# Optimization experiments

Measured on AMD Instinct MI355X. Metric: run time of the kernel, lower is better.

The kernel has to match this reference:

```python
import jax, jax.numpy as jnp
import numpy as np

HIDDEN = 1024

def setup_inputs() -> dict:
    key = jax.random.key(0)
    k1, k2, k3 = jax.random.split(key, 3)
    X = jax.random.normal(k1, (4, 2048, HIDDEN), dtype=jnp.float32)
    W = jax.random.normal(k2, (HIDDEN, 3 * HIDDEN), dtype=jnp.float32) * (1.0 / np.sqrt(HIDDEN))
    b = jax.random.normal(k3, (3 * HIDDEN,), dtype=jnp.float32) * 0.02
    return {"X": X, "W": W, "b": b}

def reference(X, W, b):
    D = X.shape[-1]
    # fused QKV projection: [B,S,3D]
    QKV = jnp.einsum('bsd,de->bse', X, W) + b
    Q, K, V = jnp.split(QKV, 3, axis=-1)
    # full attention scores [B,S,S]
    scores = jnp.einsum('bqd,bkd->bqk', Q, K) / jnp.sqrt(jnp.float32(D))
    attn = jax.nn.softmax(scores, axis=-1)
    out = jnp.einsum('bqk,bkd->bqd', attn, V)
    return out
```

## Files before the change

kernel.cpp:

```cpp
#include <hip/hip_runtime.h>

typedef unsigned short u16;
typedef unsigned int   u32;
typedef __attribute__((ext_vector_type(8)))  short bf16x8;
typedef __attribute__((ext_vector_type(16))) float f32x16;
typedef __attribute__((ext_vector_type(4)))  unsigned short us4;

__device__ __forceinline__ u16 f2bf(float f) {
    union { float f; u32 u; } v; v.f = f;
    u32 u = v.u;
    return (u16)((u + 0x7fffu + ((u >> 16) & 1u)) >> 16);
}
__device__ __forceinline__ float bf2f_lo(u32 p) {
    union { u32 u; float f; } t; t.u = p << 16; return t.f;
}
__device__ __forceinline__ float bf2f_hi(u32 p) {
    union { u32 u; float f; } t; t.u = p & 0xffff0000u; return t.f;
}

__device__ __forceinline__ void gload_lds16(const void* g, void* l) {
    __builtin_amdgcn_global_load_lds((const __attribute__((address_space(1))) u32*)g,
                                     (__attribute__((address_space(3))) u32*)l,
                                     16, 0, 0);
}

template<bool OUT_BF16, bool ADD_BIAS>
__global__ __launch_bounds__(256)
void gemm_bt(const u16* __restrict__ A, int lda, size_t strA,
             const u16* __restrict__ B, int ldb, size_t strB,
             void* __restrict__ Cv, int ldc, size_t strC,
             const float* __restrict__ bias, int K, float alpha)
{
    __shared__ __align__(16) u16 As[128 * 32];
    __shared__ __align__(16) u16 Bs[128 * 32];

    const int tid  = threadIdx.x;
    const int w    = tid >> 6;
    const int lane = tid & 63;
    const int wm   = w >> 1, wn = w & 1;
    const int m0   = blockIdx.y * 128, n0 = blockIdx.x * 128;
    const int l31  = lane & 31, lh = lane >> 5;

    A += (size_t)blockIdx.z * strA;
    B += (size_t)blockIdx.z * strB;

    size_t goffA[2], goffB[2];
#pragma unroll
    for (int h = 0; h < 2; ++h) {
        const int c = h * 256 + w * 64 + lane;
        const int r = c >> 2;
        const int q = ((c & 3) - (r >> 1)) & 3;
        goffA[h] = (size_t)(m0 + r) * lda + q * 8;
        goffB[h] = (size_t)(n0 + r) * ldb + q * 8;
    }

    int offA[2][2], offB[2][2];
#pragma unroll
    for (int i = 0; i < 2; ++i) {
        const int ra = wm * 64 + i * 32 + l31;
        const int rb = wn * 64 + i * 32 + l31;
#pragma unroll
        for (int ks = 0; ks < 2; ++ks) {
            const int qq = ks * 2 + lh;
            offA[i][ks] = (ra * 4 + ((qq + (ra >> 1)) & 3)) * 16;
            offB[i][ks] = (rb * 4 + ((qq + (rb >> 1)) & 3)) * 16;
        }
    }

    f32x16 acc[2][2] = {};

    for (int k0 = 0; k0 < K; k0 += 32) {
        gload_lds16(A + goffA[0] + k0, (char*)As + (w * 64) * 16);
        gload_lds16(A + goffA[1] + k0, (char*)As + (256 + w * 64) * 16);
        gload_lds16(B + goffB[0] + k0, (char*)Bs + (w * 64) * 16);
        gload_lds16(B + goffB[1] + k0, (char*)Bs + (256 + w * 64) * 16);
        __syncthreads();

        bf16x8 af[2][2], bfr[2][2];
#pragma unroll
        for (int i = 0; i < 2; ++i)
#pragma unroll
            for (int ks = 0; ks < 2; ++ks) {
                af[i][ks]  = *(const bf16x8*)((const char*)As + offA[i][ks]);
                bfr[i][ks] = *(const bf16x8*)((const char*)Bs + offB[i][ks]);
            }
#pragma unroll
        for (int ks = 0; ks < 2; ++ks)
#pragma unroll
            for (int i = 0; i < 2; ++i)
#pragma unroll
                for (int j = 0; j < 2; ++j)
                    acc[i][j] = __builtin_amdgcn_mfma_f32_32x32x16_bf16(
                        af[i][ks], bfr[j][ks], acc[i][j], 0, 0, 0);
        __syncthreads();
    }

    float bval[2];
    if (ADD_BIAS) {
#pragma unroll
        for (int j = 0; j < 2; ++j) bval[j] = bias[n0 + wn * 64 + j * 32 + l31];
    }
#pragma unroll
    for (int i = 0; i < 2; ++i) {
        const int rowb = m0 + wm * 64 + i * 32 + 4 * lh;
#pragma unroll
        for (int j = 0; j < 2; ++j) {
            const int col = n0 + wn * 64 + j * 32 + l31;
#pragma unroll
            for (int r = 0; r < 16; ++r) {
                const int row = rowb + (r & 3) + 8 * (r >> 2);
                float v = acc[i][j][r] * alpha;
                if (ADD_BIAS) v += bval[j];
                if (OUT_BF16)
                    ((u16*)Cv)[(size_t)blockIdx.z * strC + (size_t)row * ldc + col] = f2bf(v);
                else
                    ((float*)Cv)[(size_t)blockIdx.z * strC + (size_t)row * ldc + col] = v;
            }
        }
    }
}

__global__ __launch_bounds__(256)
void convert_x(const float* __restrict__ X, u16* __restrict__ Xb, int n4)
{
    int i = blockIdx.x * blockDim.x + threadIdx.x;
    if (i < n4) {
        float4 v = ((const float4*)X)[i];
        us4 o = { f2bf(v.x), f2bf(v.y), f2bf(v.z), f2bf(v.w) };
        ((us4*)Xb)[i] = o;
    }
}

__global__ __launch_bounds__(256)
void transpose_w(const float* __restrict__ W, u16* __restrict__ Wt)
{
    __shared__ u16 t[64][65];
    const int k0 = blockIdx.x * 64, n0 = blockIdx.y * 64;
    const int tx = threadIdx.x, ty = threadIdx.y;
#pragma unroll
    for (int i = 0; i < 64; i += 4)
        t[ty + i][tx] = f2bf(W[(size_t)(k0 + ty + i) * 3072 + n0 + tx]);
    __syncthreads();
#pragma unroll
    for (int i = 0; i < 64; i += 4)
        Wt[(size_t)(n0 + ty + i) * 1024 + k0 + tx] = t[tx][ty + i];
}

__global__ __launch_bounds__(256)
void transpose_v(const u16* __restrict__ QKV, u16* __restrict__ Vt)
{
    __shared__ u16 t[64][65];
    const int b  = blockIdx.z;
    const int d0 = blockIdx.x * 64, s0 = blockIdx.y * 64;
    const int tx = threadIdx.x, ty = threadIdx.y;
    const u16* src = QKV + (size_t)(b * 2048 + s0) * 3072 + 2048 + d0;
#pragma unroll
    for (int i = 0; i < 64; i += 4)
        t[ty + i][tx] = src[(size_t)(ty + i) * 3072 + tx];
    __syncthreads();
    u16* dst = Vt + (size_t)b * 1024 * 2048 + (size_t)d0 * 2048 + s0;
#pragma unroll
    for (int i = 0; i < 64; i += 4)
        dst[(size_t)(ty + i) * 2048 + tx] = t[tx][ty + i];
}

__global__ __launch_bounds__(256)
void softmax_rows(u16* __restrict__ S)
{
    __shared__ float redm[4], reds[4];
    u16* sr = S + (size_t)blockIdx.x * 2048;
    const int t = threadIdx.x;

    uint4 raw = ((const uint4*)sr)[t];
    float x[8];
    x[0] = bf2f_lo(raw.x); x[1] = bf2f_hi(raw.x);
    x[2] = bf2f_lo(raw.y); x[3] = bf2f_hi(raw.y);
    x[4] = bf2f_lo(raw.z); x[5] = bf2f_hi(raw.z);
    x[6] = bf2f_lo(raw.w); x[7] = bf2f_hi(raw.w);

    float mx = fmaxf(fmaxf(fmaxf(x[0], x[1]), fmaxf(x[2], x[3])),
                     fmaxf(fmaxf(x[4], x[5]), fmaxf(x[6], x[7])));
#pragma unroll
    for (int o = 32; o; o >>= 1) mx = fmaxf(mx, __shfl_xor(mx, o));
    if ((t & 63) == 0) redm[t >> 6] = mx;
    __syncthreads();
    mx = fmaxf(fmaxf(redm[0], redm[1]), fmaxf(redm[2], redm[3]));

    float e[8], s = 0.f;
#pragma unroll
    for (int k = 0; k < 8; ++k) { e[k] = __expf(x[k] - mx); s += e[k]; }
#pragma unroll
    for (int o = 32; o; o >>= 1) s += __shfl_xor(s, o);
    if ((t & 63) == 0) reds[t >> 6] = s;
    __syncthreads();
    s = reds[0] + reds[1] + reds[2] + reds[3];
    const float inv = 1.0f / s;

    uint4 o4;
    o4.x = (u32)f2bf(e[0] * inv) | ((u32)f2bf(e[1] * inv) << 16);
    o4.y = (u32)f2bf(e[2] * inv) | ((u32)f2bf(e[3] * inv) << 16);
    o4.z = (u32)f2bf(e[4] * inv) | ((u32)f2bf(e[5] * inv) << 16);
    o4.w = (u32)f2bf(e[6] * inv) | ((u32)f2bf(e[7] * inv) << 16);
    ((uint4*)sr)[t] = o4;
}

extern "C" void kernel_launch(void* const* d_in, const int* in_sizes, int n_in,
                              void* d_out, int out_size, void* d_ws, size_t ws_size,
                              hipStream_t stream)
{
    const float* X    = (const float*)d_in[0];
    const float* W    = (const float*)d_in[1];
    const float* bias = (const float*)d_in[2];
    float* out = (float*)d_out;
    char* ws = (char*)d_ws;

    u16* QKV = (u16*)ws;
    u16* Vt  = (u16*)(ws + 50331648);
    u16* S   = (u16*)(ws + 67108864);
    u16* Xb  = (u16*)(ws + 67108864);
    u16* Wt  = (u16*)(ws + 83886080);

    convert_x<<<8192, 256, 0, stream>>>(X, Xb, 8192 * 1024 / 4);
    transpose_w<<<dim3(16, 48), dim3(64, 4), 0, stream>>>(W, Wt);

    gemm_bt<true, true><<<dim3(24, 64, 1), 256, 0, stream>>>(
        Xb, 1024, 0, Wt, 1024, 0, QKV, 3072, 0, bias, 1024, 1.0f);

    transpose_v<<<dim3(16, 32, 4), dim3(64, 4), 0, stream>>>(QKV, Vt);

    gemm_bt<true, false><<<dim3(16, 16, 4), 256, 0, stream>>>(
        QKV,        3072, (size_t)2048 * 3072,
        QKV + 1024, 3072, (size_t)2048 * 3072,
        S,          2048, (size_t)2048 * 2048,
        nullptr, 1024, 0.03125f);

    softmax_rows<<<8192, 256, 0, stream>>>(S);

    gemm_bt<false, false><<<dim3(8, 16, 4), 256, 0, stream>>>(
        S,  2048, (size_t)2048 * 2048,
        Vt, 2048, (size_t)1024 * 2048,
        out, 1024, (size_t)2048 * 1024,
        nullptr, 2048, 1.0f);
}
```

Before: 287.9 us.

## Use 256x128 GEMM tiles and fuse V transpose into projection epilogue

Adds a 256x128-tile GEMM variant, where each wave computes a 128x64 sub-tile, with launch bounds allowing two blocks per CU. It is used for the QK projection and the QK^T score GEMM to raise data reuse per LDS load. The V projection is split out as its own GEMM whose epilogue writes V transposed directly, which removes the separate transpose_v kernel and its round trip of QKV through memory. The larger tiles increase register pressure and produce fewer blocks (512) for the 256-CU part, which risks lower occupancy and load imbalance.

```diff
diff --git a/kernel.cpp b/kernel.cpp
--- a/kernel.cpp
+++ b/kernel.cpp
@@ -24,9 +24,133 @@
                                      16, 0, 0);
 }
 
+template<bool OUT_BF16, bool ADD_BIAS, bool VT_OUT>
+__global__ __launch_bounds__(256, 2)
+void gemm256(const u16* __restrict__ A, int lda, size_t strA,
+             const u16* __restrict__ B, int ldb, size_t strB,
+             void* __restrict__ Cv, int ldc, size_t strC,
+             const float* __restrict__ bias, int K, float alpha)
+{
+    __shared__ __align__(16) u16 As[256 * 32];
+    __shared__ __align__(16) u16 Bs[128 * 32];
+
+    const int tid  = threadIdx.x;
+    const int w    = tid >> 6;
+    const int lane = tid & 63;
+    const int wm   = w >> 1, wn = w & 1;
+    const int m0   = blockIdx.y * 256, n0 = blockIdx.x * 128;
+    const int l31  = lane & 31, lh = lane >> 5;
+
+    A += (size_t)blockIdx.z * strA;
+    B += (size_t)blockIdx.z * strB;
+
+    size_t goffA[4], goffB[2];
+#pragma unroll
+    for (int h = 0; h < 4; ++h) {
+        const int c = h * 256 + w * 64 + lane;
+        const int r = c >> 2;
+        const int q = ((c & 3) - (r >> 1)) & 3;
+        goffA[h] = (size_t)(m0 + r) * lda + q * 8;
+    }
+#pragma unroll
+    for (int h = 0; h < 2; ++h) {
+        const int c = h * 256 + w * 64 + lane;
+        const int r = c >> 2;
+        const int q = ((c & 3) - (r >> 1)) & 3;
+        goffB[h] = (size_t)(n0 + r) * ldb + q * 8;
+    }
+
+    int offA[4][2], offB[2][2];
+#pragma unroll
+    for (int i = 0; i < 4; ++i) {
+        const int ra = wm * 128 + i * 32 + l31;
+#pragma unroll
+        for (int ks = 0; ks < 2; ++ks)
+            offA[i][ks] = (ra * 4 + ((ks * 2 + lh + (ra >> 1)) & 3)) * 16;
+    }
+#pragma unroll
+    for (int j = 0; j < 2; ++j) {
+        const int rb = wn * 64 + j * 32 + l31;
+#pragma unroll
+        for (int ks = 0; ks < 2; ++ks)
+            offB[j][ks] = (rb * 4 + ((ks * 2 + lh + (rb >> 1)) & 3)) * 16;
+    }
+
+    f32x16 acc[4][2] = {};
+
+    for (int k0 = 0; k0 < K; k0 += 32) {
+#pragma unroll
+        for (int h = 0; h < 4; ++h)
+            gload_lds16(A + goffA[h] + k0, (char*)As + (h * 256 + w * 64) * 16);
+#pragma unroll
+        for (int h = 0; h < 2; ++h)
+            gload_lds16(B + goffB[h] + k0, (char*)Bs + (h * 256 + w * 64) * 16);
+        __syncthreads();
+
+        bf16x8 af[4][2], bfr[2][2];
+#pragma unroll
+        for (int i = 0; i < 4; ++i)
+#pragma unroll
+            for (int ks = 0; ks < 2; ++ks)
+                af[i][ks] = *(const bf16x8*)((const char*)As + offA[i][ks]);
+#pragma unroll
+        for (int j = 0; j < 2; ++j)
+#pragma unroll
+            for (int ks = 0; ks < 2; ++ks)
+                bfr[j][ks] = *(const bf16x8*)((const char*)Bs + offB[j][ks]);
+
+#pragma unroll
+        for (int ks = 0; ks < 2; ++ks)
+#pragma unroll
+            for (int i = 0; i < 4; ++i)
+#pragma unroll
+                for (int j = 0; j < 2; ++j)
+                    acc[i][j] = __builtin_amdgcn_mfma_f32_32x32x16_bf16(
+                        af[i][ks], bfr[j][ks], acc[i][j], 0, 0, 0);
+        __syncthreads();
+    }
+
+    float bval[2];
+    if (ADD_BIAS) {
+#pragma unroll
+        for (int j = 0; j < 2; ++j) bval[j] = bias[n0 + wn * 64 + j * 32 + l31];
+    }
+#pragma unroll
+    for (int i = 0; i < 4; ++i) {
+        const int rowb = m0 + wm * 128 + i * 32 + 4 * lh;
+#pragma unroll
+        for (int j = 0; j < 2; ++j) {
+            const int col = n0 + wn * 64 + j * 32 + l31;
+            if (VT_OUT) {
+                const int b = rowb >> 11;
+                u16* dst = (u16*)Cv + ((size_t)(b * 1024) + col) * 2048 + (rowb & 2047);
+#pragma unroll
+                for (int g = 0; g < 4; ++g) {
+                    us4 o = { f2bf(acc[i][j][4 * g + 0] + bval[j]),
+                              f2bf(acc[i][j][4 * g + 1] + bval[j]),
+                              f2bf(acc[i][j][4 * g + 2] + bval[j]),
+                              f2bf(acc[i][j][4 * g + 3] + bval[j]) };
+                    *(us4*)(dst + 8 * g) = o;
+                }
+            } else {
+#pragma unroll
+                for (int r = 0; r < 16; ++r) {
+                    const int row = rowb + (r & 3) + 8 * (r >> 2);
+                    float v = acc[i][j][r] * alpha;
+                    if (ADD_BIAS) v += bval[j];
+                    if (OUT_BF16)
+                        ((u16*)Cv)[(size_t)blockIdx.z * strC + (size_t)row * ldc + col] = f2bf(v);
+                    else
+                        ((float*)Cv)[(size_t)blockIdx.z * strC + (size_t)row * ldc + col] = v;
+                }
+            }
+        }
+    }
+}
+
 template<bool OUT_BF16, bool ADD_BIAS>
 __global__ __launch_bounds__(256)
-void gemm_bt(const u16* __restrict__ A, int lda, size_t strA,
+void gemm128(const u16* __restrict__ A, int lda, size_t strA,
              const u16* __restrict__ B, int ldb, size_t strB,
              void* __restrict__ Cv, int ldc, size_t strC,
              const float* __restrict__ bias, int K, float alpha)
@@ -147,24 +271,6 @@
 }
 
 __global__ __launch_bounds__(256)
-void transpose_v(const u16* __restrict__ QKV, u16* __restrict__ Vt)
-{
-    __shared__ u16 t[64][65];
-    const int b  = blockIdx.z;
-    const int d0 = blockIdx.x * 64, s0 = blockIdx.y * 64;
-    const int tx = threadIdx.x, ty = threadIdx.y;
-    const u16* src = QKV + (size_t)(b * 2048 + s0) * 3072 + 2048 + d0;
-#pragma unroll
-    for (int i = 0; i < 64; i += 4)
-        t[ty + i][tx] = src[(size_t)(ty + i) * 3072 + tx];
-    __syncthreads();
-    u16* dst = Vt + (size_t)b * 1024 * 2048 + (size_t)d0 * 2048 + s0;
-#pragma unroll
-    for (int i = 0; i < 64; i += 4)
-        dst[(size_t)(ty + i) * 2048 + tx] = t[tx][ty + i];
-}
-
-__global__ __launch_bounds__(256)
 void softmax_rows(u16* __restrict__ S)
 {
     __shared__ float redm[4], reds[4];
@@ -214,29 +320,31 @@
     float* out = (float*)d_out;
     char* ws = (char*)d_ws;
 
-    u16* QKV = (u16*)ws;
-    u16* Vt  = (u16*)(ws + 50331648);
-    u16* S   = (u16*)(ws + 67108864);
-    u16* Xb  = (u16*)(ws + 67108864);
-    u16* Wt  = (u16*)(ws + 83886080);
+    u16* QK = (u16*)ws;
+    u16* Vt = (u16*)(ws + 33554432);
+    u16* S  = (u16*)(ws + 50331648);
+    u16* Xb = (u16*)(ws + 50331648);
+    u16* Wt = (u16*)(ws + 67108864);
 
     convert_x<<<8192, 256, 0, stream>>>(X, Xb, 8192 * 1024 / 4);
     transpose_w<<<dim3(16, 48), dim3(64, 4), 0, stream>>>(W, Wt);
 
-    gemm_bt<true, true><<<dim3(24, 64, 1), 256, 0, stream>>>(
-        Xb, 1024, 0, Wt, 1024, 0, QKV, 3072, 0, bias, 1024, 1.0f);
-
-    transpose_v<<<dim3(16, 32, 4), dim3(64, 4), 0, stream>>>(QKV, Vt);
-
-    gemm_bt<true, false><<<dim3(16, 16, 4), 256, 0, stream>>>(
-        QKV,        3072, (size_t)2048 * 3072,
-        QKV + 1024, 3072, (size_t)2048 * 3072,
-        S,          2048, (size_t)2048 * 2048,
+    gemm256<true, true, false><<<dim3(16, 32, 1), 256, 0, stream>>>(
+        Xb, 1024, 0, Wt, 1024, 0, QK, 2048, 0, bias, 1024, 1.0f);
+
+    gemm256<true, true, true><<<dim3(8, 32, 1), 256, 0, stream>>>(
+        Xb, 1024, 0, Wt + (size_t)2048 * 1024, 1024, 0, Vt, 2048, 0,
+        bias + 2048, 1024, 1.0f);
+
+    gemm256<true, false, false><<<dim3(16, 8, 4), 256, 0, stream>>>(
+        QK,        2048, (size_t)2048 * 2048,
+        QK + 1024, 2048, (size_t)2048 * 2048,
+        S,         2048, (size_t)2048 * 2048,
         nullptr, 1024, 0.03125f);
 
     softmax_rows<<<8192, 256, 0, stream>>>(S);
 
-    gemm_bt<false, false><<<dim3(8, 16, 4), 256, 0, stream>>>(
+    gemm128<false, false><<<dim3(8, 16, 4), 256, 0, stream>>>(
         S,  2048, (size_t)2048 * 2048,
         Vt, 2048, (size_t)1024 * 2048,
         out, 1024, (size_t)2048 * 1024,
```

Result: no change. 287.0 us (-0.3%).
